# Kernel optimization log

Hardware: AMD Instinct MI355X
Metric: run time of the kernel (lower is better)

## Reference

```python
import jax, jax.numpy as jnp
import numpy as np

N_NODES = 50000
N_EDGES = 800000
NUM_RELATIONS = 8   # 2 * n_speakers**2 with n_speakers = 2
NUM_BASES = 30
G_DIM, H1_DIM, H2_DIM = 128, 128, 128


def setup_inputs() -> dict:
    key = jax.random.key(0)
    ks = jax.random.split(key, 10)
    inp = {
        "node_features": jax.random.normal(ks[0], (N_NODES, G_DIM), jnp.float32),
        "edge_index": jax.random.randint(ks[1], (2, N_EDGES), 0, N_NODES, dtype=jnp.int64),
        "edge_type": jax.random.randint(ks[2], (N_EDGES,), 0, NUM_RELATIONS, dtype=jnp.int64),
        "edge_norm": jax.random.uniform(ks[3], (N_EDGES,), jnp.float32),
        # RGCNConv params (basis decomposition)
        "basis": jax.random.normal(ks[4], (NUM_BASES, G_DIM, H1_DIM), jnp.float32) * 0.05,
        "comp": jax.random.normal(ks[5], (NUM_RELATIONS, NUM_BASES), jnp.float32) * 0.1,
        "root": jax.random.normal(ks[6], (G_DIM, H1_DIM), jnp.float32) * 0.05,
        "bias1": jnp.zeros((H1_DIM,), jnp.float32),
        # GraphConv params: lin_rel (with bias) applied to aggregated neighbors, lin_root (no bias)
        "w_rel": jax.random.normal(ks[7], (H1_DIM, H2_DIM), jnp.float32) * 0.05,
        "b_rel": jnp.zeros((H2_DIM,), jnp.float32),
        "w_root": jax.random.normal(ks[8], (H1_DIM, H2_DIM), jnp.float32) * 0.05,
    }
    return inp


def reference(node_features, edge_index, edge_type, edge_norm,
              basis, comp, root, bias1, w_rel, b_rel, w_root):
    src, dst = edge_index[0], edge_index[1]  # source_to_target flow (PyG default)

    # ---- Layer 1: RGCNConv with basis decomposition ----
    # W[r] = sum_b comp[r,b] * basis[b]  -> [R, g, h1]
    W = jnp.einsum('rb,bio->rio', comp, basis)
    # Project every node under every relation once (N*R*h1), then gather per edge.
    # Mathematically identical to per-edge x_j @ W[edge_type] but avoids an [E, g, h1] tensor.
    x_proj = jnp.einsum('ni,rio->nro', node_features, W)  # [N, R, h1]
    msg = x_proj[src, edge_type] * edge_norm[:, None]     # [E, h1]
    agg = jax.ops.segment_sum(msg, dst, num_segments=N_NODES)  # scatter-add to targets
    h = agg + node_features @ root + bias1                # [N, h1]

    # ---- Layer 2: GraphConv (aggr='add', no edge_weight) ----
    agg2 = jax.ops.segment_sum(h[src], dst, num_segments=N_NODES)  # [N, h1]
    out = agg2 @ w_rel + b_rel + h @ w_root               # [N, h2]
    return out
```

## Files before the change

kernel.cpp:

```cpp
#include <hip/hip_runtime.h>
#include <hip/hip_bf16.h>
#include <stdint.h>

#define N_NODES 50000
#define N_EDGES 800000
#define NREL    8
#define NBASES  30
#define DIM     128
#define NSLOT   9
#define NCAT    (NSLOT*DIM)
#define SCAN_NB ((N_NODES + 255) / 256)
#define NB_C    196
#define EPB_PLACE 2048
#define NBLK_PLACE ((N_EDGES + EPB_PLACE - 1) / EPB_PLACE)
#define GEMMH_TILES ((N_NODES + 63) / 64)
#define PREP_TOTAL  (NCAT * DIM + 2 * DIM * DIM)
#define PREP_BLKS   ((PREP_TOTAL + 255) / 256)
#define CONV_BLKS   ((N_NODES * DIM / 4 + 255) / 256)
#define HIST_BLKS   ((N_EDGES + 255) / 256)

typedef __attribute__((ext_vector_type(8))) short short8;
typedef __attribute__((ext_vector_type(4))) float floatx4;
typedef __hip_bfloat16  bf16;
typedef __hip_bfloat162 bf16x2;

__device__ inline ushort f2bu(float f) { bf16 b = __float2bfloat16(f); return *(ushort*)&b; }
__device__ inline float  bu2f(ushort u) { union { unsigned i; float f; } c; c.i = ((unsigned)u) << 16; return c.f; }

__global__ __launch_bounds__(256) void setup_kernel(const float* __restrict__ basis, const float* __restrict__ comp,
                                                    const float* __restrict__ root, const float* __restrict__ w_rel,
                                                    const float* __restrict__ w_root,
                                                    bf16* __restrict__ W2T, bf16* __restrict__ wrelT,
                                                    bf16* __restrict__ wrootT,
                                                    const float4* __restrict__ x4, ushort4* __restrict__ xb4,
                                                    const int* __restrict__ ei, int* __restrict__ deg) {
    int b = blockIdx.x;
    if (b < PREP_BLKS) {
        int idx = b * 256 + threadIdx.x;
        const int n_cat = NCAT * DIM;
        const int n_sq  = DIM * DIM;
        if (idx < n_cat) {
            int o = idx / NCAT;
            int rem = idx - o * NCAT;
            int r = rem >> 7, k = rem & 127;
            float v;
            if (r < NREL) {
                v = 0.f;
                for (int bb = 0; bb < NBASES; ++bb)
                    v += comp[r * NBASES + bb] * basis[(bb * DIM + k) * DIM + o];
            } else {
                v = root[k * DIM + o];
            }
            W2T[idx] = __float2bfloat16(v);
        } else if (idx < n_cat + n_sq) {
            int t = idx - n_cat; int k = t & 127, o = t >> 7;
            wrelT[o * DIM + k] = __float2bfloat16(w_rel[k * DIM + o]);
        } else if (idx < n_cat + 2 * n_sq) {
            int t = idx - n_cat - n_sq; int k = t & 127, o = t >> 7;
            wrootT[o * DIM + k] = __float2bfloat16(w_root[k * DIM + o]);
        }
    } else if (b < PREP_BLKS + CONV_BLKS) {
        int i = (b - PREP_BLKS) * 256 + threadIdx.x;
        int n4 = N_NODES * DIM / 4;
        if (i < n4) {
            float4 f = x4[i];
            ushort4 o;
            o.x = f2bu(f.x); o.y = f2bu(f.y); o.z = f2bu(f.z); o.w = f2bu(f.w);
            xb4[i] = o;
        }
    } else {
        int e = (b - PREP_BLKS - CONV_BLKS) * 256 + threadIdx.x;
        if (e < N_EDGES) atomicAdd(&deg[ei[N_EDGES + e]], 1);
    }
}

__global__ __launch_bounds__(256) void scan_one(const int* __restrict__ deg, int* __restrict__ segoff,
                                                unsigned long long* __restrict__ bstate, int n) {
    __shared__ int buf[256];
    int b = blockIdx.x, tid = threadIdx.x;
    int i = b * 256 + tid;
    int v = (i < n) ? deg[i] : 0;
    buf[tid] = v;
    __syncthreads();
#pragma unroll
    for (int o = 1; o < 256; o <<= 1) {
        int t = (tid >= o) ? buf[tid - o] : 0;
        __syncthreads();
        buf[tid] += t;
        __syncthreads();
    }
    int incl = buf[tid];
    int total = buf[255];
    if (tid == 0)
        __hip_atomic_store(&bstate[b], (1ULL << 32) | (unsigned)total,
                           __ATOMIC_RELEASE, __HIP_MEMORY_SCOPE_AGENT);
    int mysum = 0;
    for (int j = tid; j < b; j += 256) {
        unsigned long long s;
        do {
            s = __hip_atomic_load(&bstate[j], __ATOMIC_ACQUIRE, __HIP_MEMORY_SCOPE_AGENT);
        } while (!(s >> 32));
        mysum += (int)(s & 0xFFFFFFFFu);
    }
    __syncthreads();
    buf[tid] = mysum;
    __syncthreads();
#pragma unroll
    for (int o = 128; o > 0; o >>= 1) {
        if (tid < o) buf[tid] += buf[tid + o];
        __syncthreads();
    }
    int base = buf[0];
    if (i < n) segoff[i + 1] = base + incl;
    if (b == 0 && tid == 0) segoff[0] = 0;
}

__global__ __launch_bounds__(256) void place_kernel(const int* __restrict__ ei, const int* __restrict__ et,
                                                    const float* __restrict__ en, const int* __restrict__ segoff,
                                                    int* __restrict__ bcur, uint2* __restrict__ tmp) {
    __shared__ int lhist[NB_C];
    __shared__ int lbase[NB_C];
    __shared__ int lrank[NB_C];
    int tid = threadIdx.x;
    for (int i = tid; i < NB_C; i += 256) { lhist[i] = 0; lrank[i] = 0; }
    __syncthreads();
    int e0 = blockIdx.x * EPB_PLACE;
#pragma unroll
    for (int i = 0; i < EPB_PLACE / 256; ++i) {
        int e = e0 + i * 256 + tid;
        if (e < N_EDGES) atomicAdd(&lhist[ei[N_EDGES + e] >> 8], 1);
    }
    __syncthreads();
    for (int c = tid; c < NB_C; c += 256)
        if (lhist[c] > 0) lbase[c] = atomicAdd(&bcur[c], lhist[c]);
    __syncthreads();
#pragma unroll
    for (int i = 0; i < EPB_PLACE / 256; ++i) {
        int e = e0 + i * 256 + tid;
        if (e < N_EDGES) {
            int d = ei[N_EDGES + e];
            int c = d >> 8;
            int r = atomicAdd(&lrank[c], 1);
            int p = segoff[c << 8] + lbase[c] + r;
            tmp[p] = make_uint2((unsigned)ei[e] | ((unsigned)et[e] << 16) | ((unsigned)(d & 255) << 19),
                                __float_as_uint(en[e]));
        }
    }
}

__global__ __launch_bounds__(256) void sortb_kernel(const uint2* __restrict__ tmp, const int* __restrict__ segoff,
                                                    uint2* __restrict__ rec) {
    __shared__ int hist2[256 * 8];
    int c = blockIdx.x;
    int tid = threadIdx.x;
    for (int i = tid; i < 256 * 8; i += 256) hist2[i] = 0;
    __syncthreads();
    int base = segoff[c << 8];
    int nlimit = (c + 1) << 8; if (nlimit > N_NODES) nlimit = N_NODES;
    int end = segoff[nlimit];
    for (int i = base + tid; i < end; i += 256) {
        unsigned x = tmp[i].x;
        int dl = (x >> 19) & 255, ty = (x >> 16) & 7;
        atomicAdd(&hist2[dl * 8 + ty], 1);
    }
    __syncthreads();
    {
        int node = (c << 8) + tid;
        int run = (node < N_NODES) ? (segoff[node] - base) : 0;
#pragma unroll
        for (int t = 0; t < 8; ++t) {
            int cnt = hist2[tid * 8 + t];
            hist2[tid * 8 + t] = run;
            run += cnt;
        }
    }
    __syncthreads();
    for (int i = base + tid; i < end; i += 256) {
        uint2 r = tmp[i];
        int dl = (r.x >> 19) & 255, ty = (r.x >> 16) & 7;
        int p = base + atomicAdd(&hist2[dl * 8 + ty], 1);
        rec[p] = make_uint2(r.x & 0x7FFFFu, r.y);
    }
}

__device__ inline void flush8(ushort* dst, const float* acc) {
    short8 o;
#pragma unroll
    for (int f = 0; f < 8; ++f) o[f] = (short)f2bu(acc[f]);
    *(short8*)dst = o;
}

__global__ void gath1_kernel(const uint2* __restrict__ rec, const int* __restrict__ segoff,
                             const ushort* __restrict__ xb, ushort* __restrict__ s) {
    int quad = threadIdx.x >> 4;
    int node = blockIdx.x * 16 + quad;
    if (node >= N_NODES) return;
    int lane = threadIdx.x & 15;
    ushort* sp = s + (size_t)node * NCAT + lane * 8;
    int st = segoff[node], en = segoff[node + 1];
    float acc[8] = {0.f, 0.f, 0.f, 0.f, 0.f, 0.f, 0.f, 0.f};
    int cur = -1;
    unsigned mask = 0;
    for (int chunk = st; chunk < en; chunk += 4) {
        int m = en - chunk; if (m > 4) m = 4;
        uint2 rr[4]; short8 vv[4];
#pragma unroll
        for (int j = 0; j < 4; ++j) if (j < m) rr[j] = rec[chunk + j];
#pragma unroll
        for (int j = 0; j < 4; ++j) if (j < m)
            vv[j] = *(const short8*)(xb + (size_t)(rr[j].x & 0xFFFFu) * 128 + lane * 8);
#pragma unroll
        for (int j = 0; j < 4; ++j) if (j < m) {
            int ty = (int)(rr[j].x >> 16);
            if (ty != cur) {
                if (cur >= 0) flush8(sp + cur * 128, acc);
                cur = ty;
                mask |= 1u << ty;
#pragma unroll
                for (int f = 0; f < 8; ++f) acc[f] = 0.f;
            }
            float nrm = __uint_as_float(rr[j].y);
#pragma unroll
            for (int f = 0; f < 8; ++f) acc[f] += nrm * bu2f((ushort)vv[j][f]);
        }
    }
    if (cur >= 0) flush8(sp + cur * 128, acc);
    short8 z = {0, 0, 0, 0, 0, 0, 0, 0};
#pragma unroll
    for (int t = 0; t < 8; ++t)
        if (!(mask & (1u << t))) *(short8*)(sp + t * 128) = z;
    *(short8*)(sp + 8 * 128) = *(const short8*)(xb + (size_t)node * 128 + lane * 8);
}

__global__ __launch_bounds__(256) void gemmh_kernel(const bf16* __restrict__ S, const bf16* __restrict__ B2T,
                                                    const float* __restrict__ bias1, bf16* __restrict__ H, int M) {
    __shared__ ushort As[64][136];
    __shared__ ushort Bs[128][136];
    const ushort* Su = (const ushort*)S;
    const ushort* Bu = (const ushort*)B2T;
    ushort* Hu = (ushort*)H;
    int tm = blockIdx.x * 64;
    int wave = threadIdx.x >> 6, lane = threadIdx.x & 63;
    int q = lane >> 4, mr = lane & 15;
    floatx4 zero = {0.f, 0.f, 0.f, 0.f};
    floatx4 acc[8] = {zero, zero, zero, zero, zero, zero, zero, zero};

    for (int ch = 0; ch < 9; ++ch) {
        if (ch) __syncthreads();
#pragma unroll
        for (int u = 0; u < 4; ++u) {
            int cc = threadIdx.x + u * 256;
            int row = cc >> 4, seg = cc & 15;
            int gr = tm + row;
            short8 av = {0, 0, 0, 0, 0, 0, 0, 0};
            if (gr < M) av = *(const short8*)(Su + (size_t)gr * NCAT + ch * 128 + seg * 8);
            *(short8*)(&As[row][seg * 8]) = av;
        }
#pragma unroll
        for (int u = 0; u < 8; ++u) {
            int cc = threadIdx.x + u * 256;
            int row = cc >> 4, seg = cc & 15;
            short8 bv = *(const short8*)(Bu + (size_t)row * NCAT + ch * 128 + seg * 8);
            *(short8*)(&Bs[row][seg * 8]) = bv;
        }
        __syncthreads();
#pragma unroll
        for (int kt = 0; kt < 4; ++kt) {
            short8 a = *(const short8*)(&As[wave * 16 + mr][q * 8 + kt * 32]);
#pragma unroll
            for (int nt = 0; nt < 8; ++nt) {
                short8 b = *(const short8*)(&Bs[nt * 16 + mr][q * 8 + kt * 32]);
                acc[nt] = __builtin_amdgcn_mfma_f32_16x16x32_bf16(a, b, acc[nt], 0, 0, 0);
            }
        }
    }
#pragma unroll
    for (int nt = 0; nt < 8; ++nt) {
        float bi = bias1[nt * 16 + mr];
#pragma unroll
        for (int r4 = 0; r4 < 4; ++r4) {
            int row = tm + wave * 16 + q * 4 + r4;
            if (row < M) Hu[(size_t)row * 128 + nt * 16 + mr] = f2bu(acc[nt][r4] + bi);
        }
    }
}

__global__ void seg2_kernel(const uint2* __restrict__ rec, const int* __restrict__ segoff,
                            const ushort* __restrict__ h, ushort* __restrict__ out2) {
    int quad = threadIdx.x >> 4;
    int node = blockIdx.x * 16 + quad;
    if (node >= N_NODES) return;
    int lane = threadIdx.x & 15;
    int st = segoff[node], en = segoff[node + 1];
    float acc[8] = {0.f, 0.f, 0.f, 0.f, 0.f, 0.f, 0.f, 0.f};
    for (int chunk = st; chunk < en; chunk += 4) {
        int m = en - chunk; if (m > 4) m = 4;
        uint2 rr[4]; short8 vv[4];
#pragma unroll
        for (int j = 0; j < 4; ++j) if (j < m) rr[j] = rec[chunk + j];
#pragma unroll
        for (int j = 0; j < 4; ++j) if (j < m)
            vv[j] = *(const short8*)(h + (size_t)(rr[j].x & 0xFFFFu) * 128 + lane * 8);
#pragma unroll
        for (int j = 0; j < 4; ++j) if (j < m)
#pragma unroll
            for (int f = 0; f < 8; ++f) acc[f] += bu2f((ushort)vv[j][f]);
    }
    short8 o;
#pragma unroll
    for (int f = 0; f < 8; ++f) o[f] = (short)f2bu(acc[f]);
    *(short8*)(out2 + (size_t)node * 128 + lane * 8) = o;
}

__global__ __launch_bounds__(256) void gemm2_kernel(const bf16* __restrict__ A1, const bf16* __restrict__ B1T,
                                                    const bf16* __restrict__ A2, const bf16* __restrict__ B2T,
                                                    const float* __restrict__ brel, float* __restrict__ out, int M) {
    __shared__ ushort As[64][136];
    __shared__ ushort Bs[64][136];
    int tm = blockIdx.x * 64, tn = blockIdx.y * 64;
    int wave = threadIdx.x >> 6, lane = threadIdx.x & 63;
    int q = lane >> 4, mr = lane & 15;
    floatx4 zero = {0.f, 0.f, 0.f, 0.f};
    floatx4 acc[4] = {zero, zero, zero, zero};

    for (int phase = 0; phase < 2; ++phase) {
        const ushort* Au = (const ushort*)(phase ? A2 : A1);
        const ushort* Bu = (const ushort*)(phase ? B2T : B1T);
        if (phase) __syncthreads();
        for (int c = threadIdx.x; c < 64 * 16; c += 256) {
            int row = c >> 4, seg = c & 15;
            int gr = tm + row;
            short8 av = {0, 0, 0, 0, 0, 0, 0, 0};
            if (gr < M) av = *(const short8*)(Au + (size_t)gr * 128 + seg * 8);
            *(short8*)(&As[row][seg * 8]) = av;
            short8 bv = *(const short8*)(Bu + (size_t)(tn + row) * 128 + seg * 8);
            *(short8*)(&Bs[row][seg * 8]) = bv;
        }
        __syncthreads();
#pragma unroll
        for (int kt = 0; kt < 4; ++kt) {
            short8 a = *(const short8*)(&As[wave * 16 + mr][q * 8 + kt * 32]);
#pragma unroll
            for (int nt = 0; nt < 4; ++nt) {
                short8 b = *(const short8*)(&Bs[nt * 16 + mr][q * 8 + kt * 32]);
                acc[nt] = __builtin_amdgcn_mfma_f32_16x16x32_bf16(a, b, acc[nt], 0, 0, 0);
            }
        }
    }
    __syncthreads();
    float* Csf = (float*)&As[0][0];
#pragma unroll
    for (int nt = 0; nt < 4; ++nt)
#pragma unroll
        for (int r4 = 0; r4 < 4; ++r4) {
            int row = wave * 16 + q * 4 + r4;
            int col = nt * 16 + mr;
            Csf[row * 68 + col] = acc[nt][r4] + brel[tn + col];
        }
    __syncthreads();
#pragma unroll
    for (int u = 0; u < 4; ++u) {
        int cc = threadIdx.x + u * 256;
        int row = cc >> 4, seg = cc & 15;
        int gr = tm + row;
        if (gr < M) {
            float4 v = *(const float4*)(&Csf[row * 68 + seg * 4]);
            *(float4*)(out + (size_t)gr * 128 + tn + seg * 4) = v;
        }
    }
}

extern "C" void kernel_launch(void* const* d_in, const int* in_sizes, int n_in,
                              void* d_out, int out_size, void* d_ws, size_t ws_size,
                              hipStream_t stream) {
    const float* x      = (const float*)d_in[0];
    const int*   ei     = (const int*)d_in[1];
    const int*   et     = (const int*)d_in[2];
    const float* en     = (const float*)d_in[3];
    const float* basis  = (const float*)d_in[4];
    const float* comp   = (const float*)d_in[5];
    const float* root   = (const float*)d_in[6];
    const float* bias1  = (const float*)d_in[7];
    const float* w_rel  = (const float*)d_in[8];
    const float* b_rel  = (const float*)d_in[9];
    const float* w_root = (const float*)d_in[10];
    float* out = (float*)d_out;

    char* ws = (char*)d_ws;
    size_t off = 0;
    auto alloc = [&](size_t bytes) { size_t o = off; off += (bytes + 255) & ~(size_t)255; return o; };

    size_t o_deg    = alloc((size_t)N_NODES * 4);
    size_t o_bcur   = alloc((size_t)NB_C * 4);
    size_t o_bstate = alloc((size_t)SCAN_NB * 8);
    size_t o_segoff = alloc((size_t)(N_NODES + 1) * 4);
    size_t o_rec    = alloc((size_t)N_EDGES * 8);
    size_t o_tmp    = alloc((size_t)N_EDGES * 8);
    size_t o_w2t    = alloc((size_t)NCAT * DIM * 2);
    size_t o_wrel   = alloc((size_t)DIM * DIM * 2);
    size_t o_wroot  = alloc((size_t)DIM * DIM * 2);
    size_t o_xb     = alloc((size_t)N_NODES * DIM * 2);
    size_t o_s      = alloc((size_t)N_NODES * NCAT * 2);
    size_t o_hb     = alloc((size_t)N_NODES * DIM * 2);
    size_t o_agg2   = alloc((size_t)N_NODES * DIM * 2);

    int*   deg    = (int*)(ws + o_deg);
    int*   bcur   = (int*)(ws + o_bcur);
    unsigned long long* bstate = (unsigned long long*)(ws + o_bstate);
    int*   segoff = (int*)(ws + o_segoff);
    uint2* rec    = (uint2*)(ws + o_rec);
    uint2* tmp    = (uint2*)(ws + o_tmp);
    bf16*  w2t    = (bf16*)(ws + o_w2t);
    bf16*  wrelT  = (bf16*)(ws + o_wrel);
    bf16*  wrootT = (bf16*)(ws + o_wroot);
    bf16*  xb     = (bf16*)(ws + o_xb);
    bf16*  sbuf   = (bf16*)(ws + o_s);
    bf16*  hb     = (bf16*)(ws + o_hb);
    bf16*  agg2   = (bf16*)(ws + o_agg2);

    hipMemsetAsync(ws + o_deg, 0, o_segoff - o_deg, stream);

    setup_kernel<<<PREP_BLKS + CONV_BLKS + HIST_BLKS, 256, 0, stream>>>(
        basis, comp, root, w_rel, w_root, w2t, wrelT, wrootT,
        (const float4*)x, (ushort4*)xb, ei, deg);
    scan_one<<<SCAN_NB, 256, 0, stream>>>(deg, segoff, bstate, N_NODES);
    place_kernel<<<NBLK_PLACE, 256, 0, stream>>>(ei, et, en, segoff, bcur, tmp);
    sortb_kernel<<<NB_C, 256, 0, stream>>>(tmp, segoff, rec);
    gath1_kernel<<<(N_NODES + 15) / 16, 256, 0, stream>>>(rec, segoff, (const ushort*)xb, (ushort*)sbuf);
    gemmh_kernel<<<GEMMH_TILES, 256, 0, stream>>>(sbuf, w2t, bias1, hb, N_NODES);
    seg2_kernel<<<(N_NODES + 15) / 16, 256, 0, stream>>>(rec, segoff, (const ushort*)hb, (ushort*)agg2);
    {
        dim3 grid((N_NODES + 63) / 64, DIM / 64);
        gemm2_kernel<<<grid, 256, 0, stream>>>(agg2, wrelT, hb, wrootT, b_rel, out, N_NODES);
    }
}
```

Before: 350.5 us.

## Fuse edge gathers into the GEMM tiles, removing intermediate S and agg2 buffers

The per-relation gather of neighbor features is now computed directly into the GEMM's shared-memory A tile, using per-node per-type offsets written by the sort kernel. This removes the 115 MB bf16 intermediate S buffer that was written and then re-read. Layer 2 likewise folds the neighbor sum, the lin_rel GEMM and the root GEMM into one kernel, dropping agg2 and using full-width 128-column tiles. In exchange, gather latency is now serialized with the MFMA work inside each block, with only 782 blocks and heavy LDS use per block, so there is less parallelism available to hide the irregular loads.

```diff
diff --git a/kernel.cpp b/kernel.cpp
--- a/kernel.cpp
+++ b/kernel.cpp
@@ -13,7 +13,7 @@
 #define NB_C    196
 #define EPB_PLACE 2048
 #define NBLK_PLACE ((N_EDGES + EPB_PLACE - 1) / EPB_PLACE)
-#define GEMMH_TILES ((N_NODES + 63) / 64)
+#define ROW_TILES ((N_NODES + 63) / 64)
 #define PREP_TOTAL  (NCAT * DIM + 2 * DIM * DIM)
 #define PREP_BLKS   ((PREP_TOTAL + 255) / 256)
 #define CONV_BLKS   ((N_NODES * DIM / 4 + 255) / 256)
@@ -149,7 +149,7 @@
 }
 
 __global__ __launch_bounds__(256) void sortb_kernel(const uint2* __restrict__ tmp, const int* __restrict__ segoff,
-                                                    uint2* __restrict__ rec) {
+                                                    uint2* __restrict__ rec, int* __restrict__ typeoff) {
     __shared__ int hist2[256 * 8];
     int c = blockIdx.x;
     int tid = threadIdx.x;
@@ -166,12 +166,18 @@
     __syncthreads();
     {
         int node = (c << 8) + tid;
-        int run = (node < N_NODES) ? (segoff[node] - base) : 0;
-#pragma unroll
-        for (int t = 0; t < 8; ++t) {
-            int cnt = hist2[tid * 8 + t];
-            hist2[tid * 8 + t] = run;
-            run += cnt;
+        if (node < N_NODES) {
+            int run = segoff[node] - base;
+            int offs[8];
+#pragma unroll
+            for (int t = 0; t < 8; ++t) {
+                int cnt = hist2[tid * 8 + t];
+                hist2[tid * 8 + t] = run;
+                offs[t] = base + run;
+                run += cnt;
+            }
+            *(int4*)(typeoff + (size_t)node * 8)     = make_int4(offs[0], offs[1], offs[2], offs[3]);
+            *(int4*)(typeoff + (size_t)node * 8 + 4) = make_int4(offs[4], offs[5], offs[6], offs[7]);
         }
     }
     __syncthreads();
@@ -190,78 +196,59 @@
     *(short8*)dst = o;
 }
 
-__global__ void gath1_kernel(const uint2* __restrict__ rec, const int* __restrict__ segoff,
-                             const ushort* __restrict__ xb, ushort* __restrict__ s) {
-    int quad = threadIdx.x >> 4;
-    int node = blockIdx.x * 16 + quad;
-    if (node >= N_NODES) return;
-    int lane = threadIdx.x & 15;
-    ushort* sp = s + (size_t)node * NCAT + lane * 8;
-    int st = segoff[node], en = segoff[node + 1];
-    float acc[8] = {0.f, 0.f, 0.f, 0.f, 0.f, 0.f, 0.f, 0.f};
-    int cur = -1;
-    unsigned mask = 0;
-    for (int chunk = st; chunk < en; chunk += 4) {
-        int m = en - chunk; if (m > 4) m = 4;
-        uint2 rr[4]; short8 vv[4];
-#pragma unroll
-        for (int j = 0; j < 4; ++j) if (j < m) rr[j] = rec[chunk + j];
-#pragma unroll
-        for (int j = 0; j < 4; ++j) if (j < m)
-            vv[j] = *(const short8*)(xb + (size_t)(rr[j].x & 0xFFFFu) * 128 + lane * 8);
-#pragma unroll
-        for (int j = 0; j < 4; ++j) if (j < m) {
-            int ty = (int)(rr[j].x >> 16);
-            if (ty != cur) {
-                if (cur >= 0) flush8(sp + cur * 128, acc);
-                cur = ty;
-                mask |= 1u << ty;
-#pragma unroll
-                for (int f = 0; f < 8; ++f) acc[f] = 0.f;
-            }
-            float nrm = __uint_as_float(rr[j].y);
-#pragma unroll
-            for (int f = 0; f < 8; ++f) acc[f] += nrm * bu2f((ushort)vv[j][f]);
-        }
-    }
-    if (cur >= 0) flush8(sp + cur * 128, acc);
-    short8 z = {0, 0, 0, 0, 0, 0, 0, 0};
-#pragma unroll
-    for (int t = 0; t < 8; ++t)
-        if (!(mask & (1u << t))) *(short8*)(sp + t * 128) = z;
-    *(short8*)(sp + 8 * 128) = *(const short8*)(xb + (size_t)node * 128 + lane * 8);
-}
-
-__global__ __launch_bounds__(256) void gemmh_kernel(const bf16* __restrict__ S, const bf16* __restrict__ B2T,
-                                                    const float* __restrict__ bias1, bf16* __restrict__ H, int M) {
+__global__ __launch_bounds__(256) void rgcn1_kernel(const uint2* __restrict__ rec, const int* __restrict__ typeoff,
+                                                    const int* __restrict__ segoff, const ushort* __restrict__ xb,
+                                                    const ushort* __restrict__ W2Tu, const float* __restrict__ bias1,
+                                                    ushort* __restrict__ H) {
     __shared__ ushort As[64][136];
     __shared__ ushort Bs[128][136];
-    const ushort* Su = (const ushort*)S;
-    const ushort* Bu = (const ushort*)B2T;
-    ushort* Hu = (ushort*)H;
     int tm = blockIdx.x * 64;
-    int wave = threadIdx.x >> 6, lane = threadIdx.x & 63;
+    int tid = threadIdx.x;
+    int wave = tid >> 6, lane = tid & 63;
     int q = lane >> 4, mr = lane & 15;
+    int quad = tid >> 4, kl = tid & 15;
     floatx4 zero = {0.f, 0.f, 0.f, 0.f};
     floatx4 acc[8] = {zero, zero, zero, zero, zero, zero, zero, zero};
 
     for (int ch = 0; ch < 9; ++ch) {
         if (ch) __syncthreads();
 #pragma unroll
-        for (int u = 0; u < 4; ++u) {
-            int cc = threadIdx.x + u * 256;
+        for (int u = 0; u < 8; ++u) {
+            int cc = tid + u * 256;
             int row = cc >> 4, seg = cc & 15;
-            int gr = tm + row;
-            short8 av = {0, 0, 0, 0, 0, 0, 0, 0};
-            if (gr < M) av = *(const short8*)(Su + (size_t)gr * NCAT + ch * 128 + seg * 8);
-            *(short8*)(&As[row][seg * 8]) = av;
-        }
-#pragma unroll
-        for (int u = 0; u < 8; ++u) {
-            int cc = threadIdx.x + u * 256;
-            int row = cc >> 4, seg = cc & 15;
-            short8 bv = *(const short8*)(Bu + (size_t)row * NCAT + ch * 128 + seg * 8);
-            *(short8*)(&Bs[row][seg * 8]) = bv;
+            *(short8*)(&Bs[row][seg * 8]) = *(const short8*)(W2Tu + (size_t)row * NCAT + ch * 128 + seg * 8);
+        }
+#pragma unroll
+        for (int rd = 0; rd < 4; ++rd) {
+            int nl = rd * 16 + quad;
+            int node = tm + nl;
+            if (ch == 8) {
+                short8 v = {0, 0, 0, 0, 0, 0, 0, 0};
+                if (node < N_NODES) v = *(const short8*)(xb + (size_t)node * 128 + kl * 8);
+                *(short8*)(&As[nl][kl * 8]) = v;
+            } else {
+                float a8[8] = {0.f, 0.f, 0.f, 0.f, 0.f, 0.f, 0.f, 0.f};
+                if (node < N_NODES) {
+                    int st = typeoff[(size_t)node * 8 + ch];
+                    int en = (ch < 7) ? typeoff[(size_t)node * 8 + ch + 1] : segoff[node + 1];
+                    for (int eo = st; eo < en; eo += 4) {
+                        int m = en - eo; if (m > 4) m = 4;
+                        uint2 rr[4]; short8 vv[4];
+#pragma unroll
+                        for (int j = 0; j < 4; ++j) if (j < m) rr[j] = rec[eo + j];
+#pragma unroll
+                        for (int j = 0; j < 4; ++j) if (j < m)
+                            vv[j] = *(const short8*)(xb + (size_t)(rr[j].x & 0xFFFFu) * 128 + kl * 8);
+#pragma unroll
+                        for (int j = 0; j < 4; ++j) if (j < m) {
+                            float nrm = __uint_as_float(rr[j].y);
+#pragma unroll
+                            for (int f = 0; f < 8; ++f) a8[f] += nrm * bu2f((ushort)vv[j][f]);
+                        }
+                    }
+                }
+                flush8(&As[nl][kl * 8], a8);
+            }
         }
         __syncthreads();
 #pragma unroll
@@ -280,92 +267,115 @@
 #pragma unroll
         for (int r4 = 0; r4 < 4; ++r4) {
             int row = tm + wave * 16 + q * 4 + r4;
-            if (row < M) Hu[(size_t)row * 128 + nt * 16 + mr] = f2bu(acc[nt][r4] + bi);
-        }
-    }
-}
-
-__global__ void seg2_kernel(const uint2* __restrict__ rec, const int* __restrict__ segoff,
-                            const ushort* __restrict__ h, ushort* __restrict__ out2) {
-    int quad = threadIdx.x >> 4;
-    int node = blockIdx.x * 16 + quad;
-    if (node >= N_NODES) return;
-    int lane = threadIdx.x & 15;
-    int st = segoff[node], en = segoff[node + 1];
-    float acc[8] = {0.f, 0.f, 0.f, 0.f, 0.f, 0.f, 0.f, 0.f};
-    for (int chunk = st; chunk < en; chunk += 4) {
-        int m = en - chunk; if (m > 4) m = 4;
-        uint2 rr[4]; short8 vv[4];
-#pragma unroll
-        for (int j = 0; j < 4; ++j) if (j < m) rr[j] = rec[chunk + j];
-#pragma unroll
-        for (int j = 0; j < 4; ++j) if (j < m)
-            vv[j] = *(const short8*)(h + (size_t)(rr[j].x & 0xFFFFu) * 128 + lane * 8);
-#pragma unroll
-        for (int j = 0; j < 4; ++j) if (j < m)
-#pragma unroll
-            for (int f = 0; f < 8; ++f) acc[f] += bu2f((ushort)vv[j][f]);
-    }
-    short8 o;
-#pragma unroll
-    for (int f = 0; f < 8; ++f) o[f] = (short)f2bu(acc[f]);
-    *(short8*)(out2 + (size_t)node * 128 + lane * 8) = o;
-}
-
-__global__ __launch_bounds__(256) void gemm2_kernel(const bf16* __restrict__ A1, const bf16* __restrict__ B1T,
-                                                    const bf16* __restrict__ A2, const bf16* __restrict__ B2T,
-                                                    const float* __restrict__ brel, float* __restrict__ out, int M) {
+            if (row < N_NODES) H[(size_t)row * 128 + nt * 16 + mr] = f2bu(acc[nt][r4] + bi);
+        }
+    }
+}
+
+__global__ __launch_bounds__(256) void rgcn2_kernel(const uint2* __restrict__ rec, const int* __restrict__ segoff,
+                                                    const ushort* __restrict__ h, const ushort* __restrict__ wrelTu,
+                                                    const ushort* __restrict__ wrootTu, const float* __restrict__ brel,
+                                                    float* __restrict__ out) {
     __shared__ ushort As[64][136];
-    __shared__ ushort Bs[64][136];
-    int tm = blockIdx.x * 64, tn = blockIdx.y * 64;
-    int wave = threadIdx.x >> 6, lane = threadIdx.x & 63;
+    __shared__ ushort Bs[128][136];
+    int tm = blockIdx.x * 64;
+    int tid = threadIdx.x;
+    int wave = tid >> 6, lane = tid & 63;
     int q = lane >> 4, mr = lane & 15;
+    int quad = tid >> 4, kl = tid & 15;
     floatx4 zero = {0.f, 0.f, 0.f, 0.f};
-    floatx4 acc[4] = {zero, zero, zero, zero};
-
-    for (int phase = 0; phase < 2; ++phase) {
-        const ushort* Au = (const ushort*)(phase ? A2 : A1);
-        const ushort* Bu = (const ushort*)(phase ? B2T : B1T);
-        if (phase) __syncthreads();
-        for (int c = threadIdx.x; c < 64 * 16; c += 256) {
-            int row = c >> 4, seg = c & 15;
-            int gr = tm + row;
-            short8 av = {0, 0, 0, 0, 0, 0, 0, 0};
-            if (gr < M) av = *(const short8*)(Au + (size_t)gr * 128 + seg * 8);
-            *(short8*)(&As[row][seg * 8]) = av;
-            short8 bv = *(const short8*)(Bu + (size_t)(tn + row) * 128 + seg * 8);
-            *(short8*)(&Bs[row][seg * 8]) = bv;
-        }
-        __syncthreads();
-#pragma unroll
-        for (int kt = 0; kt < 4; ++kt) {
-            short8 a = *(const short8*)(&As[wave * 16 + mr][q * 8 + kt * 32]);
-#pragma unroll
-            for (int nt = 0; nt < 4; ++nt) {
-                short8 b = *(const short8*)(&Bs[nt * 16 + mr][q * 8 + kt * 32]);
-                acc[nt] = __builtin_amdgcn_mfma_f32_16x16x32_bf16(a, b, acc[nt], 0, 0, 0);
-            }
-        }
-    }
-    __syncthreads();
-    float* Csf = (float*)&As[0][0];
-#pragma unroll
-    for (int nt = 0; nt < 4; ++nt)
-#pragma unroll
-        for (int r4 = 0; r4 < 4; ++r4) {
-            int row = wave * 16 + q * 4 + r4;
-            int col = nt * 16 + mr;
-            Csf[row * 68 + col] = acc[nt][r4] + brel[tn + col];
-        }
-    __syncthreads();
+    floatx4 acc[8] = {zero, zero, zero, zero, zero, zero, zero, zero};
+
+#pragma unroll
+    for (int u = 0; u < 8; ++u) {
+        int cc = tid + u * 256;
+        int row = cc >> 4, seg = cc & 15;
+        *(short8*)(&Bs[row][seg * 8]) = *(const short8*)(wrelTu + (size_t)row * 128 + seg * 8);
+    }
+#pragma unroll
+    for (int rd = 0; rd < 4; ++rd) {
+        int nl = rd * 16 + quad;
+        int node = tm + nl;
+        float a8[8] = {0.f, 0.f, 0.f, 0.f, 0.f, 0.f, 0.f, 0.f};
+        if (node < N_NODES) {
+            int st = segoff[node], en = segoff[node + 1];
+            for (int eo = st; eo < en; eo += 4) {
+                int m = en - eo; if (m > 4) m = 4;
+                uint2 rr[4]; short8 vv[4];
+#pragma unroll
+                for (int j = 0; j < 4; ++j) if (j < m) rr[j] = rec[eo + j];
+#pragma unroll
+                for (int j = 0; j < 4; ++j) if (j < m)
+                    vv[j] = *(const short8*)(h + (size_t)(rr[j].x & 0xFFFFu) * 128 + kl * 8);
+#pragma unroll
+                for (int j = 0; j < 4; ++j) if (j < m)
+#pragma unroll
+                    for (int f = 0; f < 8; ++f) a8[f] += bu2f((ushort)vv[j][f]);
+            }
+        }
+        flush8(&As[nl][kl * 8], a8);
+    }
+    __syncthreads();
+#pragma unroll
+    for (int kt = 0; kt < 4; ++kt) {
+        short8 a = *(const short8*)(&As[wave * 16 + mr][q * 8 + kt * 32]);
+#pragma unroll
+        for (int nt = 0; nt < 8; ++nt) {
+            short8 b = *(const short8*)(&Bs[nt * 16 + mr][q * 8 + kt * 32]);
+            acc[nt] = __builtin_amdgcn_mfma_f32_16x16x32_bf16(a, b, acc[nt], 0, 0, 0);
+        }
+    }
+    __syncthreads();
+#pragma unroll
+    for (int u = 0; u < 8; ++u) {
+        int cc = tid + u * 256;
+        int row = cc >> 4, seg = cc & 15;
+        *(short8*)(&Bs[row][seg * 8]) = *(const short8*)(wrootTu + (size_t)row * 128 + seg * 8);
+    }
 #pragma unroll
     for (int u = 0; u < 4; ++u) {
-        int cc = threadIdx.x + u * 256;
+        int cc = tid + u * 256;
         int row = cc >> 4, seg = cc & 15;
         int gr = tm + row;
-        if (gr < M) {
-            float4 v = *(const float4*)(&Csf[row * 68 + seg * 4]);
-            *(float4*)(out + (size_t)gr * 128 + tn + seg * 4) = v;
+        short8 av = {0, 0, 0, 0, 0, 0, 0, 0};
+        if (gr < N_NODES) av = *(const short8*)(h + (size_t)gr * 128 + seg * 8);
+        *(short8*)(&As[row][seg * 8]) = av;
+    }
+    __syncthreads();
+#pragma unroll
+    for (int kt = 0; kt < 4; ++kt) {
+        short8 a = *(const short8*)(&As[wave * 16 + mr][q * 8 + kt * 32]);
+#pragma unroll
+        for (int nt = 0; nt < 8; ++nt) {
+            short8 b = *(const short8*)(&Bs[nt * 16 + mr][q * 8 + kt * 32]);
+            acc[nt] = __builtin_amdgcn_mfma_f32_16x16x32_bf16(a, b, acc[nt], 0, 0, 0);
+        }
+    }
+    __syncthreads();
+    float* Csf = (float*)&As[0][0];
+    for (int half = 0; half < 2; ++half) {
+        if (half) __syncthreads();
+#pragma unroll
+        for (int nt = 0; nt < 4; ++nt) {
+            int nt2 = half * 4 + nt;
+            int col = nt2 * 16 + mr;
+            float bi = brel[col];
+#pragma unroll
+            for (int r4 = 0; r4 < 4; ++r4) {
+                int row = wave * 16 + q * 4 + r4;
+                Csf[row * 68 + col - half * 64] = acc[nt2][r4] + bi;
+            }
+        }
+        __syncthreads();
+#pragma unroll
+        for (int u = 0; u < 4; ++u) {
+            int cc = tid + u * 256;
+            int row = cc >> 4, seg = cc & 15;
+            int gr = tm + row;
+            if (gr < N_NODES) {
+                float4 v = *(const float4*)(&Csf[row * 68 + seg * 4]);
+                *(float4*)(out + (size_t)gr * 128 + half * 64 + seg * 4) = v;
+            }
         }
     }
 }
@@ -394,29 +404,27 @@
     size_t o_bcur   = alloc((size_t)NB_C * 4);
     size_t o_bstate = alloc((size_t)SCAN_NB * 8);
     size_t o_segoff = alloc((size_t)(N_NODES + 1) * 4);
+    size_t o_toff   = alloc((size_t)N_NODES * 8 * 4);
     size_t o_rec    = alloc((size_t)N_EDGES * 8);
     size_t o_tmp    = alloc((size_t)N_EDGES * 8);
     size_t o_w2t    = alloc((size_t)NCAT * DIM * 2);
     size_t o_wrel   = alloc((size_t)DIM * DIM * 2);
     size_t o_wroot  = alloc((size_t)DIM * DIM * 2);
     size_t o_xb     = alloc((size_t)N_NODES * DIM * 2);
-    size_t o_s      = alloc((size_t)N_NODES * NCAT * 2);
     size_t o_hb     = alloc((size_t)N_NODES * DIM * 2);
-    size_t o_agg2   = alloc((size_t)N_NODES * DIM * 2);
 
     int*   deg    = (int*)(ws + o_deg);
     int*   bcur   = (int*)(ws + o_bcur);
     unsigned long long* bstate = (unsigned long long*)(ws + o_bstate);
     int*   segoff = (int*)(ws + o_segoff);
+    int*   toff   = (int*)(ws + o_toff);
     uint2* rec    = (uint2*)(ws + o_rec);
     uint2* tmp    = (uint2*)(ws + o_tmp);
     bf16*  w2t    = (bf16*)(ws + o_w2t);
     bf16*  wrelT  = (bf16*)(ws + o_wrel);
     bf16*  wrootT = (bf16*)(ws + o_wroot);
     bf16*  xb     = (bf16*)(ws + o_xb);
-    bf16*  sbuf   = (bf16*)(ws + o_s);
     bf16*  hb     = (bf16*)(ws + o_hb);
-    bf16*  agg2   = (bf16*)(ws + o_agg2);
 
     hipMemsetAsync(ws + o_deg, 0, o_segoff - o_deg, stream);
 
@@ -425,12 +433,9 @@
         (const float4*)x, (ushort4*)xb, ei, deg);
     scan_one<<<SCAN_NB, 256, 0, stream>>>(deg, segoff, bstate, N_NODES);
     place_kernel<<<NBLK_PLACE, 256, 0, stream>>>(ei, et, en, segoff, bcur, tmp);
-    sortb_kernel<<<NB_C, 256, 0, stream>>>(tmp, segoff, rec);
-    gath1_kernel<<<(N_NODES + 15) / 16, 256, 0, stream>>>(rec, segoff, (const ushort*)xb, (ushort*)sbuf);
-    gemmh_kernel<<<GEMMH_TILES, 256, 0, stream>>>(sbuf, w2t, bias1, hb, N_NODES);
-    seg2_kernel<<<(N_NODES + 15) / 16, 256, 0, stream>>>(rec, segoff, (const ushort*)hb, (ushort*)agg2);
-    {
-        dim3 grid((N_NODES + 63) / 64, DIM / 64);
-        gemm2_kernel<<<grid, 256, 0, stream>>>(agg2, wrelT, hb, wrootT, b_rel, out, N_NODES);
-    }
-}
+    sortb_kernel<<<NB_C, 256, 0, stream>>>(tmp, segoff, rec, toff);
+    rgcn1_kernel<<<ROW_TILES, 256, 0, stream>>>(rec, toff, segoff, (const ushort*)xb,
+                                                (const ushort*)w2t, bias1, (ushort*)hb);
+    rgcn2_kernel<<<ROW_TILES, 256, 0, stream>>>(rec, segoff, (const ushort*)hb,
+                                                (const ushort*)wrelT, (const ushort*)wrootT, b_rel, out);
+}
```

Result: slower. 458.8 us (+30.9%).

## Fuse per-relation gather with layer-1 GEMM, keeping concatenated rows in LDS

Applied to the files above, without the earlier changes.

Merges the per-relation gather kernel and the layer-1 GEMM into one kernel. Each block gathers 32 nodes' 9x128 concatenated features into shared memory and multiplies them by the stacked weights with MFMA, reading B directly from global memory. sortb now writes per-node, per-type edge offsets, so the gather walks each relation segment without tracking type changes. This removes the ~115 MB intermediate S buffer write and re-read, at the cost of a large LDS footprint (about 74 KB per block) and B being re-read from L2 by every block.

```diff
diff --git a/kernel.cpp b/kernel.cpp
--- a/kernel.cpp
+++ b/kernel.cpp
@@ -13,7 +13,9 @@
 #define NB_C    196
 #define EPB_PLACE 2048
 #define NBLK_PLACE ((N_EDGES + EPB_PLACE - 1) / EPB_PLACE)
-#define GEMMH_TILES ((N_NODES + 63) / 64)
+#define M_T1    32
+#define T1_BLOCKS ((N_NODES + M_T1 - 1) / M_T1)
+#define APAD    1160
 #define PREP_TOTAL  (NCAT * DIM + 2 * DIM * DIM)
 #define PREP_BLKS   ((PREP_TOTAL + 255) / 256)
 #define CONV_BLKS   ((N_NODES * DIM / 4 + 255) / 256)
@@ -149,7 +151,7 @@
 }
 
 __global__ __launch_bounds__(256) void sortb_kernel(const uint2* __restrict__ tmp, const int* __restrict__ segoff,
-                                                    uint2* __restrict__ rec) {
+                                                    uint2* __restrict__ rec, int* __restrict__ typeoff) {
     __shared__ int hist2[256 * 8];
     int c = blockIdx.x;
     int tid = threadIdx.x;
@@ -166,12 +168,18 @@
     __syncthreads();
     {
         int node = (c << 8) + tid;
-        int run = (node < N_NODES) ? (segoff[node] - base) : 0;
-#pragma unroll
-        for (int t = 0; t < 8; ++t) {
-            int cnt = hist2[tid * 8 + t];
-            hist2[tid * 8 + t] = run;
-            run += cnt;
+        if (node < N_NODES) {
+            int run = segoff[node] - base;
+            int offs[8];
+#pragma unroll
+            for (int t = 0; t < 8; ++t) {
+                int cnt = hist2[tid * 8 + t];
+                hist2[tid * 8 + t] = run;
+                offs[t] = base + run;
+                run += cnt;
+            }
+            *(int4*)(typeoff + (size_t)node * 8)     = make_int4(offs[0], offs[1], offs[2], offs[3]);
+            *(int4*)(typeoff + (size_t)node * 8 + 4) = make_int4(offs[4], offs[5], offs[6], offs[7]);
         }
     }
     __syncthreads();
@@ -190,99 +198,74 @@
     *(short8*)dst = o;
 }
 
-__global__ void gath1_kernel(const uint2* __restrict__ rec, const int* __restrict__ segoff,
-                             const ushort* __restrict__ xb, ushort* __restrict__ s) {
-    int quad = threadIdx.x >> 4;
-    int node = blockIdx.x * 16 + quad;
-    if (node >= N_NODES) return;
-    int lane = threadIdx.x & 15;
-    ushort* sp = s + (size_t)node * NCAT + lane * 8;
-    int st = segoff[node], en = segoff[node + 1];
-    float acc[8] = {0.f, 0.f, 0.f, 0.f, 0.f, 0.f, 0.f, 0.f};
-    int cur = -1;
-    unsigned mask = 0;
-    for (int chunk = st; chunk < en; chunk += 4) {
-        int m = en - chunk; if (m > 4) m = 4;
-        uint2 rr[4]; short8 vv[4];
-#pragma unroll
-        for (int j = 0; j < 4; ++j) if (j < m) rr[j] = rec[chunk + j];
-#pragma unroll
-        for (int j = 0; j < 4; ++j) if (j < m)
-            vv[j] = *(const short8*)(xb + (size_t)(rr[j].x & 0xFFFFu) * 128 + lane * 8);
-#pragma unroll
-        for (int j = 0; j < 4; ++j) if (j < m) {
-            int ty = (int)(rr[j].x >> 16);
-            if (ty != cur) {
-                if (cur >= 0) flush8(sp + cur * 128, acc);
-                cur = ty;
-                mask |= 1u << ty;
-#pragma unroll
-                for (int f = 0; f < 8; ++f) acc[f] = 0.f;
+__global__ __launch_bounds__(512, 4) void rgcn1_kernel(const uint2* __restrict__ rec, const int* __restrict__ typeoff,
+                                                       const int* __restrict__ segoff, const ushort* __restrict__ xb,
+                                                       const ushort* __restrict__ W2Tu, const float* __restrict__ bias1,
+                                                       ushort* __restrict__ H) {
+    __shared__ ushort As[M_T1][APAD];
+    int tm = blockIdx.x * M_T1;
+    int tid = threadIdx.x;
+    int quad = tid >> 4, kl = tid & 15;
+    int node = tm + quad;
+
+    int offs[10];
+    if (node < N_NODES) {
+        int4 o0 = *(const int4*)(typeoff + (size_t)node * 8);
+        int4 o1 = *(const int4*)(typeoff + (size_t)node * 8 + 4);
+        offs[0] = o0.x; offs[1] = o0.y; offs[2] = o0.z; offs[3] = o0.w;
+        offs[4] = o1.x; offs[5] = o1.y; offs[6] = o1.z; offs[7] = o1.w;
+        offs[8] = segoff[node + 1];
+    } else {
+#pragma unroll
+        for (int t = 0; t < 9; ++t) offs[t] = 0;
+    }
+#pragma unroll
+    for (int t = 0; t < 8; ++t) {
+        float a8[8] = {0.f, 0.f, 0.f, 0.f, 0.f, 0.f, 0.f, 0.f};
+        for (int eo = offs[t]; eo < offs[t + 1]; eo += 4) {
+            int m = offs[t + 1] - eo; if (m > 4) m = 4;
+            uint2 rr[4]; short8 vv[4];
+#pragma unroll
+            for (int j = 0; j < 4; ++j) if (j < m) rr[j] = rec[eo + j];
+#pragma unroll
+            for (int j = 0; j < 4; ++j) if (j < m)
+                vv[j] = *(const short8*)(xb + (size_t)(rr[j].x & 0xFFFFu) * 128 + kl * 8);
+#pragma unroll
+            for (int j = 0; j < 4; ++j) if (j < m) {
+                float nrm = __uint_as_float(rr[j].y);
+#pragma unroll
+                for (int f = 0; f < 8; ++f) a8[f] += nrm * bu2f((ushort)vv[j][f]);
             }
-            float nrm = __uint_as_float(rr[j].y);
-#pragma unroll
-            for (int f = 0; f < 8; ++f) acc[f] += nrm * bu2f((ushort)vv[j][f]);
-        }
-    }
-    if (cur >= 0) flush8(sp + cur * 128, acc);
-    short8 z = {0, 0, 0, 0, 0, 0, 0, 0};
-#pragma unroll
-    for (int t = 0; t < 8; ++t)
-        if (!(mask & (1u << t))) *(short8*)(sp + t * 128) = z;
-    *(short8*)(sp + 8 * 128) = *(const short8*)(xb + (size_t)node * 128 + lane * 8);
-}
-
-__global__ __launch_bounds__(256) void gemmh_kernel(const bf16* __restrict__ S, const bf16* __restrict__ B2T,
-                                                    const float* __restrict__ bias1, bf16* __restrict__ H, int M) {
-    __shared__ ushort As[64][136];
-    __shared__ ushort Bs[128][136];
-    const ushort* Su = (const ushort*)S;
-    const ushort* Bu = (const ushort*)B2T;
-    ushort* Hu = (ushort*)H;
-    int tm = blockIdx.x * 64;
-    int wave = threadIdx.x >> 6, lane = threadIdx.x & 63;
+        }
+        flush8(&As[quad][t * 128 + kl * 8], a8);
+    }
+    {
+        short8 v = {0, 0, 0, 0, 0, 0, 0, 0};
+        if (node < N_NODES) v = *(const short8*)(xb + (size_t)node * 128 + kl * 8);
+        *(short8*)(&As[quad][8 * 128 + kl * 8]) = v;
+    }
+    __syncthreads();
+
+    int wave = tid >> 6, lane = tid & 63;
     int q = lane >> 4, mr = lane & 15;
     floatx4 zero = {0.f, 0.f, 0.f, 0.f};
-    floatx4 acc[8] = {zero, zero, zero, zero, zero, zero, zero, zero};
-
-    for (int ch = 0; ch < 9; ++ch) {
-        if (ch) __syncthreads();
-#pragma unroll
-        for (int u = 0; u < 4; ++u) {
-            int cc = threadIdx.x + u * 256;
-            int row = cc >> 4, seg = cc & 15;
-            int gr = tm + row;
-            short8 av = {0, 0, 0, 0, 0, 0, 0, 0};
-            if (gr < M) av = *(const short8*)(Su + (size_t)gr * NCAT + ch * 128 + seg * 8);
-            *(short8*)(&As[row][seg * 8]) = av;
-        }
-#pragma unroll
-        for (int u = 0; u < 8; ++u) {
-            int cc = threadIdx.x + u * 256;
-            int row = cc >> 4, seg = cc & 15;
-            short8 bv = *(const short8*)(Bu + (size_t)row * NCAT + ch * 128 + seg * 8);
-            *(short8*)(&Bs[row][seg * 8]) = bv;
-        }
-        __syncthreads();
-#pragma unroll
-        for (int kt = 0; kt < 4; ++kt) {
-            short8 a = *(const short8*)(&As[wave * 16 + mr][q * 8 + kt * 32]);
-#pragma unroll
-            for (int nt = 0; nt < 8; ++nt) {
-                short8 b = *(const short8*)(&Bs[nt * 16 + mr][q * 8 + kt * 32]);
-                acc[nt] = __builtin_amdgcn_mfma_f32_16x16x32_bf16(a, b, acc[nt], 0, 0, 0);
-            }
-        }
-    }
-#pragma unroll
-    for (int nt = 0; nt < 8; ++nt) {
-        float bi = bias1[nt * 16 + mr];
+    floatx4 acc[2] = {zero, zero};
+    const ushort* brow = W2Tu + (size_t)(wave * 16 + mr) * NCAT + q * 8;
+    for (int kt = 0; kt < 36; ++kt) {
+        short8 b  = *(const short8*)(brow + kt * 32);
+        short8 a0 = *(const short8*)(&As[mr][kt * 32 + q * 8]);
+        short8 a1 = *(const short8*)(&As[16 + mr][kt * 32 + q * 8]);
+        acc[0] = __builtin_amdgcn_mfma_f32_16x16x32_bf16(a0, b, acc[0], 0, 0, 0);
+        acc[1] = __builtin_amdgcn_mfma_f32_16x16x32_bf16(a1, b, acc[1], 0, 0, 0);
+    }
+    float bi = bias1[wave * 16 + mr];
+#pragma unroll
+    for (int rt = 0; rt < 2; ++rt)
 #pragma unroll
         for (int r4 = 0; r4 < 4; ++r4) {
-            int row = tm + wave * 16 + q * 4 + r4;
-            if (row < M) Hu[(size_t)row * 128 + nt * 16 + mr] = f2bu(acc[nt][r4] + bi);
-        }
-    }
+            int row = tm + rt * 16 + q * 4 + r4;
+            if (row < N_NODES) H[(size_t)row * 128 + wave * 16 + mr] = f2bu(acc[rt][r4] + bi);
+        }
 }
 
 __global__ void seg2_kernel(const uint2* __restrict__ rec, const int* __restrict__ segoff,
@@ -394,13 +377,13 @@
     size_t o_bcur   = alloc((size_t)NB_C * 4);
     size_t o_bstate = alloc((size_t)SCAN_NB * 8);
     size_t o_segoff = alloc((size_t)(N_NODES + 1) * 4);
+    size_t o_toff   = alloc((size_t)N_NODES * 8 * 4);
     size_t o_rec    = alloc((size_t)N_EDGES * 8);
     size_t o_tmp    = alloc((size_t)N_EDGES * 8);
     size_t o_w2t    = alloc((size_t)NCAT * DIM * 2);
     size_t o_wrel   = alloc((size_t)DIM * DIM * 2);
     size_t o_wroot  = alloc((size_t)DIM * DIM * 2);
     size_t o_xb     = alloc((size_t)N_NODES * DIM * 2);
-    size_t o_s      = alloc((size_t)N_NODES * NCAT * 2);
     size_t o_hb     = alloc((size_t)N_NODES * DIM * 2);
     size_t o_agg2   = alloc((size_t)N_NODES * DIM * 2);
 
@@ -408,13 +391,13 @@
     int*   bcur   = (int*)(ws + o_bcur);
     unsigned long long* bstate = (unsigned long long*)(ws + o_bstate);
     int*   segoff = (int*)(ws + o_segoff);
+    int*   toff   = (int*)(ws + o_toff);
     uint2* rec    = (uint2*)(ws + o_rec);
     uint2* tmp    = (uint2*)(ws + o_tmp);
     bf16*  w2t    = (bf16*)(ws + o_w2t);
     bf16*  wrelT  = (bf16*)(ws + o_wrel);
     bf16*  wrootT = (bf16*)(ws + o_wroot);
     bf16*  xb     = (bf16*)(ws + o_xb);
-    bf16*  sbuf   = (bf16*)(ws + o_s);
     bf16*  hb     = (bf16*)(ws + o_hb);
     bf16*  agg2   = (bf16*)(ws + o_agg2);
 
@@ -425,9 +408,9 @@
         (const float4*)x, (ushort4*)xb, ei, deg);
     scan_one<<<SCAN_NB, 256, 0, stream>>>(deg, segoff, bstate, N_NODES);
     place_kernel<<<NBLK_PLACE, 256, 0, stream>>>(ei, et, en, segoff, bcur, tmp);
-    sortb_kernel<<<NB_C, 256, 0, stream>>>(tmp, segoff, rec);
-    gath1_kernel<<<(N_NODES + 15) / 16, 256, 0, stream>>>(rec, segoff, (const ushort*)xb, (ushort*)sbuf);
-    gemmh_kernel<<<GEMMH_TILES, 256, 0, stream>>>(sbuf, w2t, bias1, hb, N_NODES);
+    sortb_kernel<<<NB_C, 256, 0, stream>>>(tmp, segoff, rec, toff);
+    rgcn1_kernel<<<T1_BLOCKS, 512, 0, stream>>>(rec, toff, segoff, (const ushort*)xb,
+                                                (const ushort*)w2t, bias1, (ushort*)hb);
     seg2_kernel<<<(N_NODES + 15) / 16, 256, 0, stream>>>(rec, segoff, (const ushort*)hb, (ushort*)agg2);
     {
         dim3 grid((N_NODES + 63) / 64, DIM / 64);
```

Result: slower. 367.7 us (+4.9%).
